# Kernel optimization log

Measured on AMD Instinct MI355X. Metric: run time of the kernel, lower is better.

## Reference

```python
import jax, jax.numpy as jnp
import numpy as np

B = 16384
IN = 128
H = 128
NC = 10
NATT = 3
EPS = 1e-5


def setup_inputs() -> dict:
    key = jax.random.key(0)
    ks = jax.random.split(key, 8)
    s_in = 1.0 / np.sqrt(IN)
    s_h = 1.0 / np.sqrt(H)
    return {
        "x": jax.random.normal(ks[0], (B, IN), dtype=jnp.float32),
        "W_in": jax.random.uniform(ks[1], (IN, H), jnp.float32, -s_in, s_in),
        "b_in": jax.random.uniform(ks[2], (H,), jnp.float32, -s_in, s_in),
        "W_att": jax.random.uniform(ks[3], (NATT, H, H), jnp.float32, -s_h, s_h),
        "b_att": jax.random.uniform(ks[4], (NATT, H), jnp.float32, -s_h, s_h),
        "gamma": jnp.ones((NATT, H), jnp.float32),
        "beta": jnp.zeros((NATT, H), jnp.float32),
        "W_c": jax.random.uniform(ks[5], (H, NC), jnp.float32, -s_h, s_h),
        "b_c": jax.random.uniform(ks[6], (NC,), jnp.float32, -s_h, s_h),
    }


def _layernorm(y, g, b):
    mu = jnp.mean(y, axis=-1, keepdims=True)
    var = jnp.mean((y - mu) ** 2, axis=-1, keepdims=True)
    return (y - mu) * jax.lax.rsqrt(var + EPS) * g + b


def reference(x, W_in, b_in, W_att, b_att, gamma, beta, W_c, b_c):
    # in_proj: [B, IN] -> [B, H]
    h = x @ W_in + b_in
    for i in range(NATT):
        u = jnp.tanh(h @ W_att[i] + b_att[i])            # [B, H]
        scores = u[:, :, None] * u[:, None, :]            # outer product [B, H, H]
        attn = jax.nn.softmax(scores, axis=-1)
        out = jnp.einsum("bij,bj->bi", attn, h)          # [B, H]
        h = _layernorm(h + out, gamma[i], beta[i])
    return h @ W_c + b_c                                  # [B, NC]
```

## Files before the change

kernel.cpp:

```cpp
#include <hip/hip_runtime.h>
#include <math.h>

#define B_TOT 16384
#define H     128
#define NC    10
#define NATT  3
#define TR    16
#define HBS   136
#define KT    5
#define EPS   1e-5f
#define EXM_S 100
#define EXL_S 20

typedef __attribute__((ext_vector_type(8))) short bf16x8;
typedef __attribute__((ext_vector_type(4))) float f32x4;

__device__ __forceinline__ ushort f2bf(float f) {
    union { float f; unsigned u; } v; v.f = f;
    unsigned r = v.u + 0x7fffu + ((v.u >> 16) & 1u);
    return (ushort)(r >> 16);
}

__device__ __forceinline__ float fast_tanh(float a) {
    float t = __expf(2.f * a);
    return 1.f - 2.f * __builtin_amdgcn_rcpf(t + 1.f);
}

__device__ __forceinline__ float redq(float v) {
    v += __shfl_xor(v, 16);
    v += __shfl_xor(v, 32);
    return v;
}

extern "C" __global__ __launch_bounds__(256)
void prep_weights(const float* __restrict__ W_in,
                  const float* __restrict__ W_att,
                  const float* __restrict__ W_c,
                  ushort* __restrict__ wt)
{
    int i = blockIdx.x * 256 + threadIdx.x;
    if (i < 65536) {
        int mat = i >> 14, idx = i & 16383;
        int k = idx >> 7, n = idx & 127;
        float v = (mat == 0) ? W_in[idx] : W_att[(mat - 1) * 16384 + idx];
        wt[mat * 16384 + n * H + k] = f2bf(v);
    } else if (i < 65536 + 2048) {
        int idx = i - 65536;
        int n = idx >> 7, k = idx & 127;
        float v = (n < NC) ? W_c[k * NC + n] : 0.f;
        wt[65536 + n * H + k] = f2bf(v);
    }
}

extern "C" __global__ __launch_bounds__(512, 6)
void simple_attention_kernel(const float* __restrict__ x,
                             const float* __restrict__ b_in,
                             const float* __restrict__ b_att,
                             const float* __restrict__ gamma,
                             const float* __restrict__ beta,
                             const float* __restrict__ b_c,
                             const ushort* __restrict__ wt,
                             float* __restrict__ out)
{
    __shared__ __align__(16) ushort ab[TR * HBS];
    __shared__ __align__(16) float  exm[16 * EXM_S];
    __shared__ __align__(16) float  exl[16 * EXL_S];

    const int tid  = threadIdx.x;
    const int wv   = tid >> 6;
    const int lane = tid & 63;
    const int s    = lane & 15;
    const int q    = lane >> 4;
    const int nq   = 16 * wv + 4 * q;
    const size_t rowBase = (size_t)blockIdx.x * TR;

    float h[4];
    f32x4 acc;

    if (wv < 4) {
        const float* xp = x + (rowBase + s) * H + 32 * wv + q * 8;
        float4 v0 = *(const float4*)xp;
        float4 v1 = *(const float4*)(xp + 4);
        bf16x8 a;
        a[0] = f2bf(v0.x); a[1] = f2bf(v0.y); a[2] = f2bf(v0.z); a[3] = f2bf(v0.w);
        a[4] = f2bf(v1.x); a[5] = f2bf(v1.y); a[6] = f2bf(v1.z); a[7] = f2bf(v1.w);
        *(bf16x8*)&ab[s * HBS + 32 * wv + q * 8] = a;
    }
    __syncthreads();

    {
        bf16x8 bfr[4];
        #pragma unroll
        for (int ks = 0; ks < 4; ++ks)
            bfr[ks] = *(const bf16x8*)&ab[s * HBS + ks * 32 + q * 8];
        acc = (f32x4){0.f, 0.f, 0.f, 0.f};
        #pragma unroll
        for (int ks = 0; ks < 4; ++ks) {
            bf16x8 a = *(const bf16x8*)&wt[(16 * wv + s) * H + ks * 32 + q * 8];
            acc = __builtin_amdgcn_mfma_f32_16x16x32_bf16(a, bfr[ks], acc, 0, 0, 0);
        }
        __syncthreads();
        float4 bi4 = *(const float4*)&b_in[nq];
        uint lo, hi;
        {
            float h0 = acc[0] + bi4.x, h1 = acc[1] + bi4.y;
            float h2 = acc[2] + bi4.z, h3 = acc[3] + bi4.w;
            h[0] = h0; h[1] = h1; h[2] = h2; h[3] = h3;
            lo = (uint)f2bf(h0) | ((uint)f2bf(h1) << 16);
            hi = (uint)f2bf(h2) | ((uint)f2bf(h3) << 16);
        }
        *(uint2*)&ab[s * HBS + nq] = make_uint2(lo, hi);
        __syncthreads();
    }

    const float cm[KT] = {1.00004478f, 0.99730768f, 0.49919676f, 0.17734736f, 0.04379392f};

    #pragma unroll 1
    for (int layer = 0; layer < NATT; ++layer) {
        const ushort* WT = wt + (size_t)(1 + layer) * 16384;

        bf16x8 bfr[4];
        #pragma unroll
        for (int ks = 0; ks < 4; ++ks)
            bfr[ks] = *(const bf16x8*)&ab[s * HBS + ks * 32 + q * 8];
        acc = (f32x4){0.f, 0.f, 0.f, 0.f};
        #pragma unroll
        for (int ks = 0; ks < 4; ++ks) {
            bf16x8 a = *(const bf16x8*)&WT[(16 * wv + s) * H + ks * 32 + q * 8];
            acc = __builtin_amdgcn_mfma_f32_16x16x32_bf16(a, bfr[ks], acc, 0, 0, 0);
        }
        float4 ba4 = *(const float4*)&b_att[layer * H + nq];
        float u[4];
        u[0] = fast_tanh(acc[0] + ba4.x);
        u[1] = fast_tanh(acc[1] + ba4.y);
        u[2] = fast_tanh(acc[2] + ba4.z);
        u[3] = fast_tanh(acc[3] + ba4.w);

        float m0 = 0, m1 = 0, m2 = 0, m3 = 0, m4 = 0;
        float t1 = 0, t2 = 0, t3 = 0, t4 = 0;
        #pragma unroll
        for (int r = 0; r < 4; ++r) {
            float uu = u[r], hh = h[r];
            m0 += hh;
            float p = uu;
            m1 += p * hh; t1 += p;
            p *= uu; m2 += p * hh; t2 += p;
            p *= uu; m3 += p * hh; t3 += p;
            p *= uu; m4 += p * hh; t4 += p;
        }
        m0 = redq(m0); m1 = redq(m1); m2 = redq(m2); m3 = redq(m3); m4 = redq(m4);
        t1 = redq(t1); t2 = redq(t2); t3 = redq(t3); t4 = redq(t4);
        {
            float* dst = &exm[s * EXM_S + wv * 12];
            if (q == 0)      *(f32x4*)&dst[0] = (f32x4){m0, m1, m2, m3};
            else if (q == 1) *(f32x4*)&dst[4] = (f32x4){m4, t1, t2, t3};
            else if (q == 2) *(f32x4*)&dst[8] = (f32x4){t4, 0.f, 0.f, 0.f};
        }
        __syncthreads();

        float S0, S1, S2, S3, S4, T1c, T2c, T3c, T4c;
        {
            const float* src = &exm[s * EXM_S + 24 * q];
            f32x4 a0 = *(const f32x4*)&src[0];
            f32x4 a1 = *(const f32x4*)&src[4];
            f32x4 a2 = *(const f32x4*)&src[8];
            f32x4 b0 = *(const f32x4*)&src[12];
            f32x4 b1 = *(const f32x4*)&src[16];
            f32x4 b2 = *(const f32x4*)&src[20];
            a0 += b0; a1 += b1; a2 += b2;
            S0  = redq(a0.x) * cm[0];
            S1  = redq(a0.y) * cm[1];
            S2  = redq(a0.z) * cm[2];
            S3  = redq(a0.w) * cm[3];
            S4  = redq(a1.x) * cm[4];
            T1c = redq(a1.y) * cm[1];
            T2c = redq(a1.z) * cm[2];
            T3c = redq(a1.w) * cm[3];
            T4c = redq(a2.x) * cm[4];
        }

        float ls = 0.f, lq2 = 0.f;
        #pragma unroll
        for (int r = 0; r < 4; ++r) {
            float uu = u[r];
            float num = fmaf(fmaf(fmaf(fmaf(S4, uu, S3), uu, S2), uu, S1), uu, S0);
            float den = fmaf(fmaf(fmaf(fmaf(T4c, uu, T3c), uu, T2c), uu, T1c), uu,
                             128.f * 1.00004478f);
            float yy = h[r] + num * __builtin_amdgcn_rcpf(den);
            h[r] = yy;
            ls += yy; lq2 += yy * yy;
        }
        ls  = redq(ls);
        lq2 = redq(lq2);
        if (q == 0)
            *(float2*)&exl[s * EXL_S + wv * 2] = make_float2(ls, lq2);
        __syncthreads();

        {
            f32x4 rd = *(const f32x4*)&exl[s * EXL_S + 4 * q];
            float sm  = redq(rd.x + rd.z);
            float sq2 = redq(rd.y + rd.w);
            float mu  = sm * (1.f / H);
            float var = sq2 * (1.f / H) - mu * mu;
            float inv = rsqrtf(var + EPS);
            float4 g4  = *(const float4*)&gamma[layer * H + nq];
            float4 be4 = *(const float4*)&beta [layer * H + nq];
            float h0 = (h[0] - mu) * inv * g4.x + be4.x;
            float h1 = (h[1] - mu) * inv * g4.y + be4.y;
            float h2 = (h[2] - mu) * inv * g4.z + be4.z;
            float h3 = (h[3] - mu) * inv * g4.w + be4.w;
            h[0] = h0; h[1] = h1; h[2] = h2; h[3] = h3;
            uint lo = (uint)f2bf(h0) | ((uint)f2bf(h1) << 16);
            uint hi = (uint)f2bf(h2) | ((uint)f2bf(h3) << 16);
            *(uint2*)&ab[s * HBS + nq] = make_uint2(lo, hi);
        }
        __syncthreads();
    }

    if (wv == 0) {
        const ushort* WC = wt + 4 * 16384;
        f32x4 facc = (f32x4){0.f, 0.f, 0.f, 0.f};
        #pragma unroll
        for (int ks = 0; ks < 4; ++ks) {
            bf16x8 a = *(const bf16x8*)&ab[s * HBS + ks * 32 + q * 8];
            bf16x8 b = *(const bf16x8*)&WC[s * H + ks * 32 + q * 8];
            facc = __builtin_amdgcn_mfma_f32_16x16x32_bf16(a, b, facc, 0, 0, 0);
        }
        if (s < NC) {
            float bc = b_c[s];
            #pragma unroll
            for (int r = 0; r < 4; ++r)
                out[(rowBase + 4 * q + r) * NC + s] = facc[r] + bc;
        }
    }
}

extern "C" void kernel_launch(void* const* d_in, const int* in_sizes, int n_in,
                              void* d_out, int out_size, void* d_ws, size_t ws_size,
                              hipStream_t stream) {
    const float* x     = (const float*)d_in[0];
    const float* W_in  = (const float*)d_in[1];
    const float* b_in  = (const float*)d_in[2];
    const float* W_att = (const float*)d_in[3];
    const float* b_att = (const float*)d_in[4];
    const float* gamma = (const float*)d_in[5];
    const float* beta  = (const float*)d_in[6];
    const float* W_c   = (const float*)d_in[7];
    const float* b_c   = (const float*)d_in[8];
    float* out  = (float*)d_out;
    ushort* wt  = (ushort*)d_ws;

    hipLaunchKernelGGL(prep_weights, dim3(264), dim3(256), 0, stream,
                       W_in, W_att, W_c, wt);
    hipLaunchKernelGGL(simple_attention_kernel, dim3(B_TOT / TR), dim3(512), 0, stream,
                       x, b_in, b_att, gamma, beta, b_c, wt, out);
}
```

Before: 100.6 us.

## Fold LayerNorm affine into next layer's attention weights and defer normalization

Gamma is folded into the attention weight matrices in the prep kernel, and precomputed correction vectors (gamma·W, beta·W + b_att) are stored in the workspace. The per-layer kernel now writes the un-normalized residual y to shared memory and applies mean/rstd analytically after the matmul, which removes one __syncthreads and one shared-memory round trip per layer. It adds extra prep work and reads of aux vectors, and normalizing after the bf16 matmul changes rounding behaviour because the un-normalized activations are quantized to bf16.

After: 102.8 us. +2.2%, slower.

```diff
diff --git a/kernel.cpp b/kernel.cpp
--- a/kernel.cpp
+++ b/kernel.cpp
@@ -36,26 +36,64 @@
 void prep_weights(const float* __restrict__ W_in,
                   const float* __restrict__ W_att,
                   const float* __restrict__ W_c,
+                  const float* __restrict__ gamma,
+                  const float* __restrict__ beta,
+                  const float* __restrict__ b_att,
                   ushort* __restrict__ wt)
 {
-    int i = blockIdx.x * 256 + threadIdx.x;
+    float* aux = (float*)(wt + 67584);
+    int bid = blockIdx.x;
+    if (bid >= 267) {
+        int w = (bid - 267) * 4 + (threadIdx.x >> 6);
+        if (w < 768) {
+            int l   = w >> 8;
+            int rem = w & 255;
+            int g2  = rem >> 7;
+            int n   = rem & 127;
+            int ln  = threadIdx.x & 63;
+            float sum = 0.f;
+            if (l > 0) {
+                const float* coef = (g2 == 0 ? gamma : beta) + (l - 1) * H;
+                sum = coef[ln]      * W_att[l * 16384 + ln * H + n]
+                    + coef[ln + 64] * W_att[l * 16384 + (ln + 64) * H + n];
+            }
+            #pragma unroll
+            for (int off = 1; off < 64; off <<= 1) sum += __shfl_xor(sum, off);
+            if (ln == 0) {
+                if (g2 == 1) sum += b_att[l * H + n];
+                aux[l * 512 + g2 * 128 + n] = sum;
+            }
+        }
+        return;
+    }
+    int i = bid * 256 + threadIdx.x;
     if (i < 65536) {
         int mat = i >> 14, idx = i & 16383;
         int k = idx >> 7, n = idx & 127;
         float v = (mat == 0) ? W_in[idx] : W_att[(mat - 1) * 16384 + idx];
+        if (mat >= 2) v *= gamma[(mat - 2) * H + k];
         wt[mat * 16384 + n * H + k] = f2bf(v);
-    } else if (i < 65536 + 2048) {
+    } else if (i < 67584) {
         int idx = i - 65536;
         int n = idx >> 7, k = idx & 127;
         float v = (n < NC) ? W_c[k * NC + n] : 0.f;
         wt[65536 + n * H + k] = f2bf(v);
+    } else if (i < 67584 + 768) {
+        int j = i - 67584;
+        int l = j >> 8;
+        int idx = j & 255;
+        int g = idx >> 7;
+        int n = idx & 127;
+        float v;
+        if (g == 0) v = (l == 0) ? 1.f : gamma[(l - 1) * H + n];
+        else        v = (l == 0) ? 0.f : beta [(l - 1) * H + n];
+        aux[l * 512 + (2 + g) * 128 + n] = v;
     }
 }
 
 extern "C" __global__ __launch_bounds__(512, 6)
 void simple_attention_kernel(const float* __restrict__ x,
                              const float* __restrict__ b_in,
-                             const float* __restrict__ b_att,
                              const float* __restrict__ gamma,
                              const float* __restrict__ beta,
                              const float* __restrict__ b_c,
@@ -73,8 +111,9 @@
     const int q    = lane >> 4;
     const int nq   = 16 * wv + 4 * q;
     const size_t rowBase = (size_t)blockIdx.x * TR;
-
-    float h[4];
+    const float* aux = (const float*)(wt + 67584);
+
+    float y[4];
     f32x4 acc;
 
     if (wv < 4) {
@@ -101,14 +140,11 @@
         }
         __syncthreads();
         float4 bi4 = *(const float4*)&b_in[nq];
-        uint lo, hi;
-        {
-            float h0 = acc[0] + bi4.x, h1 = acc[1] + bi4.y;
-            float h2 = acc[2] + bi4.z, h3 = acc[3] + bi4.w;
-            h[0] = h0; h[1] = h1; h[2] = h2; h[3] = h3;
-            lo = (uint)f2bf(h0) | ((uint)f2bf(h1) << 16);
-            hi = (uint)f2bf(h2) | ((uint)f2bf(h3) << 16);
-        }
+        float h0 = acc[0] + bi4.x, h1 = acc[1] + bi4.y;
+        float h2 = acc[2] + bi4.z, h3 = acc[3] + bi4.w;
+        y[0] = h0; y[1] = h1; y[2] = h2; y[3] = h3;
+        uint lo = (uint)f2bf(h0) | ((uint)f2bf(h1) << 16);
+        uint hi = (uint)f2bf(h2) | ((uint)f2bf(h3) << 16);
         *(uint2*)&ab[s * HBS + nq] = make_uint2(lo, hi);
         __syncthreads();
     }
@@ -118,6 +154,7 @@
     #pragma unroll 1
     for (int layer = 0; layer < NATT; ++layer) {
         const ushort* WT = wt + (size_t)(1 + layer) * 16384;
+        const float* AX  = aux + layer * 512;
 
         bf16x8 bfr[4];
         #pragma unroll
@@ -129,18 +166,38 @@
             bf16x8 a = *(const bf16x8*)&WT[(16 * wv + s) * H + ks * 32 + q * 8];
             acc = __builtin_amdgcn_mfma_f32_16x16x32_bf16(a, bfr[ks], acc, 0, 0, 0);
         }
-        float4 ba4 = *(const float4*)&b_att[layer * H + nq];
+
+        float mu, inv;
+        if (layer == 0) { mu = 0.f; inv = 1.f; }
+        else {
+            f32x4 rd = *(const f32x4*)&exl[s * EXL_S + 4 * q];
+            float sm  = redq(rd.x + rd.z);
+            float sq2 = redq(rd.y + rd.w);
+            mu  = sm * (1.f / H);
+            float var = sq2 * (1.f / H) - mu * mu;
+            inv = rsqrtf(var + EPS);
+        }
+        float invmu = inv * mu;
+
+        float4 gw4 = *(const float4*)&AX[nq];
+        float4 c14 = *(const float4*)&AX[128 + nq];
+        float4 gp4 = *(const float4*)&AX[256 + nq];
+        float4 bp4 = *(const float4*)&AX[384 + nq];
         float u[4];
-        u[0] = fast_tanh(acc[0] + ba4.x);
-        u[1] = fast_tanh(acc[1] + ba4.y);
-        u[2] = fast_tanh(acc[2] + ba4.z);
-        u[3] = fast_tanh(acc[3] + ba4.w);
+        u[0] = fast_tanh(fmaf(inv, acc[0], fmaf(-invmu, gw4.x, c14.x)));
+        u[1] = fast_tanh(fmaf(inv, acc[1], fmaf(-invmu, gw4.y, c14.y)));
+        u[2] = fast_tanh(fmaf(inv, acc[2], fmaf(-invmu, gw4.z, c14.z)));
+        u[3] = fast_tanh(fmaf(inv, acc[3], fmaf(-invmu, gw4.w, c14.w)));
+        y[0] = fmaf((y[0] - mu) * inv, gp4.x, bp4.x);
+        y[1] = fmaf((y[1] - mu) * inv, gp4.y, bp4.y);
+        y[2] = fmaf((y[2] - mu) * inv, gp4.z, bp4.z);
+        y[3] = fmaf((y[3] - mu) * inv, gp4.w, bp4.w);
 
         float m0 = 0, m1 = 0, m2 = 0, m3 = 0, m4 = 0;
         float t1 = 0, t2 = 0, t3 = 0, t4 = 0;
         #pragma unroll
         for (int r = 0; r < 4; ++r) {
-            float uu = u[r], hh = h[r];
+            float uu = u[r], hh = y[r];
             m0 += hh;
             float p = uu;
             m1 += p * hh; t1 += p;
@@ -186,35 +243,41 @@
             float num = fmaf(fmaf(fmaf(fmaf(S4, uu, S3), uu, S2), uu, S1), uu, S0);
             float den = fmaf(fmaf(fmaf(fmaf(T4c, uu, T3c), uu, T2c), uu, T1c), uu,
                              128.f * 1.00004478f);
-            float yy = h[r] + num * __builtin_amdgcn_rcpf(den);
-            h[r] = yy;
+            float yy = y[r] + num * __builtin_amdgcn_rcpf(den);
+            y[r] = yy;
             ls += yy; lq2 += yy * yy;
         }
         ls  = redq(ls);
         lq2 = redq(lq2);
-        if (q == 0)
-            *(float2*)&exl[s * EXL_S + wv * 2] = make_float2(ls, lq2);
-        __syncthreads();
-
-        {
+
+        if (layer < NATT - 1) {
+            uint lo = (uint)f2bf(y[0]) | ((uint)f2bf(y[1]) << 16);
+            uint hi = (uint)f2bf(y[2]) | ((uint)f2bf(y[3]) << 16);
+            *(uint2*)&ab[s * HBS + nq] = make_uint2(lo, hi);
+            if (q == 0)
+                *(float2*)&exl[s * EXL_S + wv * 2] = make_float2(ls, lq2);
+            __syncthreads();
+        } else {
+            if (q == 0)
+                *(float2*)&exl[s * EXL_S + wv * 2] = make_float2(ls, lq2);
+            __syncthreads();
             f32x4 rd = *(const f32x4*)&exl[s * EXL_S + 4 * q];
             float sm  = redq(rd.x + rd.z);
             float sq2 = redq(rd.y + rd.w);
-            float mu  = sm * (1.f / H);
-            float var = sq2 * (1.f / H) - mu * mu;
-            float inv = rsqrtf(var + EPS);
+            float mu2 = sm * (1.f / H);
+            float var = sq2 * (1.f / H) - mu2 * mu2;
+            float inv2 = rsqrtf(var + EPS);
             float4 g4  = *(const float4*)&gamma[layer * H + nq];
             float4 be4 = *(const float4*)&beta [layer * H + nq];
-            float h0 = (h[0] - mu) * inv * g4.x + be4.x;
-            float h1 = (h[1] - mu) * inv * g4.y + be4.y;
-            float h2 = (h[2] - mu) * inv * g4.z + be4.z;
-            float h3 = (h[3] - mu) * inv * g4.w + be4.w;
-            h[0] = h0; h[1] = h1; h[2] = h2; h[3] = h3;
+            float h0 = (y[0] - mu2) * inv2 * g4.x + be4.x;
+            float h1 = (y[1] - mu2) * inv2 * g4.y + be4.y;
+            float h2 = (y[2] - mu2) * inv2 * g4.z + be4.z;
+            float h3 = (y[3] - mu2) * inv2 * g4.w + be4.w;
             uint lo = (uint)f2bf(h0) | ((uint)f2bf(h1) << 16);
             uint hi = (uint)f2bf(h2) | ((uint)f2bf(h3) << 16);
             *(uint2*)&ab[s * HBS + nq] = make_uint2(lo, hi);
-        }
-        __syncthreads();
+            __syncthreads();
+        }
     }
 
     if (wv == 0) {
@@ -250,8 +313,8 @@
     float* out  = (float*)d_out;
     ushort* wt  = (ushort*)d_ws;
 
-    hipLaunchKernelGGL(prep_weights, dim3(264), dim3(256), 0, stream,
-                       W_in, W_att, W_c, wt);
+    hipLaunchKernelGGL(prep_weights, dim3(459), dim3(256), 0, stream,
+                       W_in, W_att, W_c, gamma, beta, b_att, wt);
     hipLaunchKernelGGL(simple_attention_kernel, dim3(B_TOT / TR), dim3(512), 0, stream,
-                       x, b_in, b_att, gamma, beta, b_c, wt, out);
-}
+                       x, b_in, gamma, beta, b_c, wt, out);
+}
```

## Process two 16-row tiles per block to reuse weight fragments across tiles

Applied to the files above, without the earlier changes.

Each block now handles 32 rows as two 16-row tiles, and each loaded weight fragment feeds two MFMAs, one per tile. This halves the global weight loads and the number of block-wide barriers per row, and gives every wave work during the input load and the classifier step. In exchange registers per thread roughly double, so the launch bound occupancy hint drops from 6 to 4, and the grid is half as large.

Result: no change. 99.08 us (median of 2 runs) (-1.5%).

```diff
diff --git a/kernel.cpp b/kernel.cpp
--- a/kernel.cpp
+++ b/kernel.cpp
@@ -5,7 +5,7 @@
 #define H     128
 #define NC    10
 #define NATT  3
-#define TR    16
+#define TRH   16
 #define HBS   136
 #define KT    5
 #define EPS   1e-5f
@@ -52,7 +52,7 @@
     }
 }
 
-extern "C" __global__ __launch_bounds__(512, 6)
+extern "C" __global__ __launch_bounds__(512, 4)
 void simple_attention_kernel(const float* __restrict__ x,
                              const float* __restrict__ b_in,
                              const float* __restrict__ b_att,
@@ -62,9 +62,9 @@
                              const ushort* __restrict__ wt,
                              float* __restrict__ out)
 {
-    __shared__ __align__(16) ushort ab[TR * HBS];
-    __shared__ __align__(16) float  exm[16 * EXM_S];
-    __shared__ __align__(16) float  exl[16 * EXL_S];
+    __shared__ __align__(16) ushort ab[2][TRH * HBS];
+    __shared__ __align__(16) float  exm[2][16 * EXM_S];
+    __shared__ __align__(16) float  exl[2][16 * EXL_S];
 
     const int tid  = threadIdx.x;
     const int wv   = tid >> 6;
@@ -72,44 +72,51 @@
     const int s    = lane & 15;
     const int q    = lane >> 4;
     const int nq   = 16 * wv + 4 * q;
-    const size_t rowBase = (size_t)blockIdx.x * TR;
-
-    float h[4];
-    f32x4 acc;
-
-    if (wv < 4) {
-        const float* xp = x + (rowBase + s) * H + 32 * wv + q * 8;
+    const size_t rowBase = (size_t)blockIdx.x * (2 * TRH);
+
+    float yA[4], yB[4];
+    f32x4 accA, accB;
+
+    {
+        int tile  = wv >> 2;
+        int slice = wv & 3;
+        const float* xp = x + (rowBase + tile * TRH + s) * H + 32 * slice + q * 8;
         float4 v0 = *(const float4*)xp;
         float4 v1 = *(const float4*)(xp + 4);
         bf16x8 a;
         a[0] = f2bf(v0.x); a[1] = f2bf(v0.y); a[2] = f2bf(v0.z); a[3] = f2bf(v0.w);
         a[4] = f2bf(v1.x); a[5] = f2bf(v1.y); a[6] = f2bf(v1.z); a[7] = f2bf(v1.w);
-        *(bf16x8*)&ab[s * HBS + 32 * wv + q * 8] = a;
+        *(bf16x8*)&ab[tile][s * HBS + 32 * slice + q * 8] = a;
     }
     __syncthreads();
 
     {
-        bf16x8 bfr[4];
-        #pragma unroll
-        for (int ks = 0; ks < 4; ++ks)
-            bfr[ks] = *(const bf16x8*)&ab[s * HBS + ks * 32 + q * 8];
-        acc = (f32x4){0.f, 0.f, 0.f, 0.f};
+        bf16x8 bfrA[4], bfrB[4];
+        #pragma unroll
+        for (int ks = 0; ks < 4; ++ks) {
+            bfrA[ks] = *(const bf16x8*)&ab[0][s * HBS + ks * 32 + q * 8];
+            bfrB[ks] = *(const bf16x8*)&ab[1][s * HBS + ks * 32 + q * 8];
+        }
+        accA = (f32x4){0.f, 0.f, 0.f, 0.f};
+        accB = (f32x4){0.f, 0.f, 0.f, 0.f};
         #pragma unroll
         for (int ks = 0; ks < 4; ++ks) {
             bf16x8 a = *(const bf16x8*)&wt[(16 * wv + s) * H + ks * 32 + q * 8];
-            acc = __builtin_amdgcn_mfma_f32_16x16x32_bf16(a, bfr[ks], acc, 0, 0, 0);
+            accA = __builtin_amdgcn_mfma_f32_16x16x32_bf16(a, bfrA[ks], accA, 0, 0, 0);
+            accB = __builtin_amdgcn_mfma_f32_16x16x32_bf16(a, bfrB[ks], accB, 0, 0, 0);
         }
         __syncthreads();
         float4 bi4 = *(const float4*)&b_in[nq];
-        uint lo, hi;
-        {
-            float h0 = acc[0] + bi4.x, h1 = acc[1] + bi4.y;
-            float h2 = acc[2] + bi4.z, h3 = acc[3] + bi4.w;
-            h[0] = h0; h[1] = h1; h[2] = h2; h[3] = h3;
-            lo = (uint)f2bf(h0) | ((uint)f2bf(h1) << 16);
-            hi = (uint)f2bf(h2) | ((uint)f2bf(h3) << 16);
-        }
-        *(uint2*)&ab[s * HBS + nq] = make_uint2(lo, hi);
+        yA[0] = accA[0] + bi4.x; yA[1] = accA[1] + bi4.y;
+        yA[2] = accA[2] + bi4.z; yA[3] = accA[3] + bi4.w;
+        yB[0] = accB[0] + bi4.x; yB[1] = accB[1] + bi4.y;
+        yB[2] = accB[2] + bi4.z; yB[3] = accB[3] + bi4.w;
+        uint loA = (uint)f2bf(yA[0]) | ((uint)f2bf(yA[1]) << 16);
+        uint hiA = (uint)f2bf(yA[2]) | ((uint)f2bf(yA[3]) << 16);
+        uint loB = (uint)f2bf(yB[0]) | ((uint)f2bf(yB[1]) << 16);
+        uint hiB = (uint)f2bf(yB[2]) | ((uint)f2bf(yB[3]) << 16);
+        *(uint2*)&ab[0][s * HBS + nq] = make_uint2(loA, hiA);
+        *(uint2*)&ab[1][s * HBS + nq] = make_uint2(loB, hiB);
         __syncthreads();
     }
 
@@ -119,48 +126,57 @@
     for (int layer = 0; layer < NATT; ++layer) {
         const ushort* WT = wt + (size_t)(1 + layer) * 16384;
 
-        bf16x8 bfr[4];
-        #pragma unroll
-        for (int ks = 0; ks < 4; ++ks)
-            bfr[ks] = *(const bf16x8*)&ab[s * HBS + ks * 32 + q * 8];
-        acc = (f32x4){0.f, 0.f, 0.f, 0.f};
+        bf16x8 bfrA[4], bfrB[4];
+        #pragma unroll
+        for (int ks = 0; ks < 4; ++ks) {
+            bfrA[ks] = *(const bf16x8*)&ab[0][s * HBS + ks * 32 + q * 8];
+            bfrB[ks] = *(const bf16x8*)&ab[1][s * HBS + ks * 32 + q * 8];
+        }
+        accA = (f32x4){0.f, 0.f, 0.f, 0.f};
+        accB = (f32x4){0.f, 0.f, 0.f, 0.f};
         #pragma unroll
         for (int ks = 0; ks < 4; ++ks) {
             bf16x8 a = *(const bf16x8*)&WT[(16 * wv + s) * H + ks * 32 + q * 8];
-            acc = __builtin_amdgcn_mfma_f32_16x16x32_bf16(a, bfr[ks], acc, 0, 0, 0);
+            accA = __builtin_amdgcn_mfma_f32_16x16x32_bf16(a, bfrA[ks], accA, 0, 0, 0);
+            accB = __builtin_amdgcn_mfma_f32_16x16x32_bf16(a, bfrB[ks], accB, 0, 0, 0);
         }
         float4 ba4 = *(const float4*)&b_att[layer * H + nq];
-        float u[4];
-        u[0] = fast_tanh(acc[0] + ba4.x);
-        u[1] = fast_tanh(acc[1] + ba4.y);
-        u[2] = fast_tanh(acc[2] + ba4.z);
-        u[3] = fast_tanh(acc[3] + ba4.w);
-
-        float m0 = 0, m1 = 0, m2 = 0, m3 = 0, m4 = 0;
-        float t1 = 0, t2 = 0, t3 = 0, t4 = 0;
-        #pragma unroll
-        for (int r = 0; r < 4; ++r) {
-            float uu = u[r], hh = h[r];
-            m0 += hh;
-            float p = uu;
-            m1 += p * hh; t1 += p;
-            p *= uu; m2 += p * hh; t2 += p;
-            p *= uu; m3 += p * hh; t3 += p;
-            p *= uu; m4 += p * hh; t4 += p;
-        }
-        m0 = redq(m0); m1 = redq(m1); m2 = redq(m2); m3 = redq(m3); m4 = redq(m4);
-        t1 = redq(t1); t2 = redq(t2); t3 = redq(t3); t4 = redq(t4);
-        {
-            float* dst = &exm[s * EXM_S + wv * 12];
+        float uA[4], uB[4];
+        uA[0] = fast_tanh(accA[0] + ba4.x); uA[1] = fast_tanh(accA[1] + ba4.y);
+        uA[2] = fast_tanh(accA[2] + ba4.z); uA[3] = fast_tanh(accA[3] + ba4.w);
+        uB[0] = fast_tanh(accB[0] + ba4.x); uB[1] = fast_tanh(accB[1] + ba4.y);
+        uB[2] = fast_tanh(accB[2] + ba4.z); uB[3] = fast_tanh(accB[3] + ba4.w);
+
+        #pragma unroll
+        for (int tl = 0; tl < 2; ++tl) {
+            const float* yy = tl ? yB : yA;
+            const float* uu = tl ? uB : uA;
+            float m0 = 0, m1 = 0, m2 = 0, m3 = 0, m4 = 0;
+            float t1 = 0, t2 = 0, t3 = 0, t4 = 0;
+            #pragma unroll
+            for (int r = 0; r < 4; ++r) {
+                float uv = uu[r], hh = yy[r];
+                m0 += hh;
+                float p = uv;
+                m1 += p * hh; t1 += p;
+                p *= uv; m2 += p * hh; t2 += p;
+                p *= uv; m3 += p * hh; t3 += p;
+                p *= uv; m4 += p * hh; t4 += p;
+            }
+            m0 = redq(m0); m1 = redq(m1); m2 = redq(m2); m3 = redq(m3); m4 = redq(m4);
+            t1 = redq(t1); t2 = redq(t2); t3 = redq(t3); t4 = redq(t4);
+            float* dst = &exm[tl][s * EXM_S + wv * 12];
             if (q == 0)      *(f32x4*)&dst[0] = (f32x4){m0, m1, m2, m3};
             else if (q == 1) *(f32x4*)&dst[4] = (f32x4){m4, t1, t2, t3};
             else if (q == 2) *(f32x4*)&dst[8] = (f32x4){t4, 0.f, 0.f, 0.f};
         }
         __syncthreads();
 
-        float S0, S1, S2, S3, S4, T1c, T2c, T3c, T4c;
-        {
-            const float* src = &exm[s * EXM_S + 24 * q];
+        #pragma unroll
+        for (int tl = 0; tl < 2; ++tl) {
+            float* yy = tl ? yB : yA;
+            const float* uu = tl ? uB : uA;
+            const float* src = &exm[tl][s * EXM_S + 24 * q];
             f32x4 a0 = *(const f32x4*)&src[0];
             f32x4 a1 = *(const f32x4*)&src[4];
             f32x4 a2 = *(const f32x4*)&src[8];
@@ -168,61 +184,63 @@
             f32x4 b1 = *(const f32x4*)&src[16];
             f32x4 b2 = *(const f32x4*)&src[20];
             a0 += b0; a1 += b1; a2 += b2;
-            S0  = redq(a0.x) * cm[0];
-            S1  = redq(a0.y) * cm[1];
-            S2  = redq(a0.z) * cm[2];
-            S3  = redq(a0.w) * cm[3];
-            S4  = redq(a1.x) * cm[4];
-            T1c = redq(a1.y) * cm[1];
-            T2c = redq(a1.z) * cm[2];
-            T3c = redq(a1.w) * cm[3];
-            T4c = redq(a2.x) * cm[4];
-        }
-
-        float ls = 0.f, lq2 = 0.f;
-        #pragma unroll
-        for (int r = 0; r < 4; ++r) {
-            float uu = u[r];
-            float num = fmaf(fmaf(fmaf(fmaf(S4, uu, S3), uu, S2), uu, S1), uu, S0);
-            float den = fmaf(fmaf(fmaf(fmaf(T4c, uu, T3c), uu, T2c), uu, T1c), uu,
-                             128.f * 1.00004478f);
-            float yy = h[r] + num * __builtin_amdgcn_rcpf(den);
-            h[r] = yy;
-            ls += yy; lq2 += yy * yy;
-        }
-        ls  = redq(ls);
-        lq2 = redq(lq2);
-        if (q == 0)
-            *(float2*)&exl[s * EXL_S + wv * 2] = make_float2(ls, lq2);
-        __syncthreads();
-
-        {
-            f32x4 rd = *(const f32x4*)&exl[s * EXL_S + 4 * q];
+            float S0  = redq(a0.x) * cm[0];
+            float S1  = redq(a0.y) * cm[1];
+            float S2  = redq(a0.z) * cm[2];
+            float S3  = redq(a0.w) * cm[3];
+            float S4  = redq(a1.x) * cm[4];
+            float T1c = redq(a1.y) * cm[1];
+            float T2c = redq(a1.z) * cm[2];
+            float T3c = redq(a1.w) * cm[3];
+            float T4c = redq(a2.x) * cm[4];
+            float ls = 0.f, lq2 = 0.f;
+            #pragma unroll
+            for (int r = 0; r < 4; ++r) {
+                float uv = uu[r];
+                float num = fmaf(fmaf(fmaf(fmaf(S4, uv, S3), uv, S2), uv, S1), uv, S0);
+                float den = fmaf(fmaf(fmaf(fmaf(T4c, uv, T3c), uv, T2c), uv, T1c), uv,
+                                 128.f * 1.00004478f);
+                float yv = yy[r] + num * __builtin_amdgcn_rcpf(den);
+                yy[r] = yv;
+                ls += yv; lq2 += yv * yv;
+            }
+            ls  = redq(ls);
+            lq2 = redq(lq2);
+            if (q == 0)
+                *(float2*)&exl[tl][s * EXL_S + wv * 2] = make_float2(ls, lq2);
+        }
+        __syncthreads();
+
+        float4 g4  = *(const float4*)&gamma[layer * H + nq];
+        float4 be4 = *(const float4*)&beta [layer * H + nq];
+        #pragma unroll
+        for (int tl = 0; tl < 2; ++tl) {
+            float* yy = tl ? yB : yA;
+            f32x4 rd = *(const f32x4*)&exl[tl][s * EXL_S + 4 * q];
             float sm  = redq(rd.x + rd.z);
             float sq2 = redq(rd.y + rd.w);
             float mu  = sm * (1.f / H);
             float var = sq2 * (1.f / H) - mu * mu;
             float inv = rsqrtf(var + EPS);
-            float4 g4  = *(const float4*)&gamma[layer * H + nq];
-            float4 be4 = *(const float4*)&beta [layer * H + nq];
-            float h0 = (h[0] - mu) * inv * g4.x + be4.x;
-            float h1 = (h[1] - mu) * inv * g4.y + be4.y;
-            float h2 = (h[2] - mu) * inv * g4.z + be4.z;
-            float h3 = (h[3] - mu) * inv * g4.w + be4.w;
-            h[0] = h0; h[1] = h1; h[2] = h2; h[3] = h3;
+            float h0 = (yy[0] - mu) * inv * g4.x + be4.x;
+            float h1 = (yy[1] - mu) * inv * g4.y + be4.y;
+            float h2 = (yy[2] - mu) * inv * g4.z + be4.z;
+            float h3 = (yy[3] - mu) * inv * g4.w + be4.w;
+            yy[0] = h0; yy[1] = h1; yy[2] = h2; yy[3] = h3;
             uint lo = (uint)f2bf(h0) | ((uint)f2bf(h1) << 16);
             uint hi = (uint)f2bf(h2) | ((uint)f2bf(h3) << 16);
-            *(uint2*)&ab[s * HBS + nq] = make_uint2(lo, hi);
-        }
-        __syncthreads();
-    }
-
-    if (wv == 0) {
+            *(uint2*)&ab[tl][s * HBS + nq] = make_uint2(lo, hi);
+        }
+        __syncthreads();
+    }
+
+    if ((wv & 3) == 0) {
+        int tile = wv >> 2;
         const ushort* WC = wt + 4 * 16384;
         f32x4 facc = (f32x4){0.f, 0.f, 0.f, 0.f};
         #pragma unroll
         for (int ks = 0; ks < 4; ++ks) {
-            bf16x8 a = *(const bf16x8*)&ab[s * HBS + ks * 32 + q * 8];
+            bf16x8 a = *(const bf16x8*)&ab[tile][s * HBS + ks * 32 + q * 8];
             bf16x8 b = *(const bf16x8*)&WC[s * H + ks * 32 + q * 8];
             facc = __builtin_amdgcn_mfma_f32_16x16x32_bf16(a, b, facc, 0, 0, 0);
         }
@@ -230,7 +248,7 @@
             float bc = b_c[s];
             #pragma unroll
             for (int r = 0; r < 4; ++r)
-                out[(rowBase + 4 * q + r) * NC + s] = facc[r] + bc;
+                out[(rowBase + tile * TRH + 4 * q + r) * NC + s] = facc[r] + bc;
         }
     }
 }
@@ -252,6 +270,6 @@
 
     hipLaunchKernelGGL(prep_weights, dim3(264), dim3(256), 0, stream,
                        W_in, W_att, W_c, wt);
-    hipLaunchKernelGGL(simple_attention_kernel, dim3(B_TOT / TR), dim3(512), 0, stream,
+    hipLaunchKernelGGL(simple_attention_kernel, dim3(B_TOT / (2 * TRH)), dim3(512), 0, stream,
                        x, b_in, b_att, gamma, beta, b_c, wt, out);
 }
```

## Use one wavefront per 16-row tile to drop cross-wave LDS reductions

Applied to the files above, without the earlier changes.

Work for a 16-row tile moves from eight wavefronts, each owning 16 output columns, to a single 64-lane wavefront that loops over all eight column tiles and keeps 32 h and u values per lane in registers. This replaces the cross-wave LDS exchanges and most block barriers for the moment sums and the layernorm statistics with in-wave shuffle reductions. The x tile is converted straight into MFMA operands without an LDS round trip. In exchange each block does eight times more serial work, uses far more registers per lane, and every wavefront reloads the full weight matrices, so latency hiding depends on enough resident waves.

Result: no change. 102.0 us (+1.4%).

```diff
diff --git a/kernel.cpp b/kernel.cpp
--- a/kernel.cpp
+++ b/kernel.cpp
@@ -5,12 +5,8 @@
 #define H     128
 #define NC    10
 #define NATT  3
-#define TR    16
 #define HBS   136
-#define KT    5
 #define EPS   1e-5f
-#define EXM_S 100
-#define EXL_S 20
 
 typedef __attribute__((ext_vector_type(8))) short bf16x8;
 typedef __attribute__((ext_vector_type(4))) float f32x4;
@@ -52,7 +48,7 @@
     }
 }
 
-extern "C" __global__ __launch_bounds__(512, 6)
+extern "C" __global__ __launch_bounds__(64)
 void simple_attention_kernel(const float* __restrict__ x,
                              const float* __restrict__ b_in,
                              const float* __restrict__ b_att,
@@ -62,58 +58,49 @@
                              const ushort* __restrict__ wt,
                              float* __restrict__ out)
 {
-    __shared__ __align__(16) ushort ab[TR * HBS];
-    __shared__ __align__(16) float  exm[16 * EXM_S];
-    __shared__ __align__(16) float  exl[16 * EXL_S];
-
-    const int tid  = threadIdx.x;
-    const int wv   = tid >> 6;
-    const int lane = tid & 63;
+    __shared__ __align__(16) ushort ab[16 * HBS];
+
+    const int lane = threadIdx.x;
     const int s    = lane & 15;
     const int q    = lane >> 4;
-    const int nq   = 16 * wv + 4 * q;
-    const size_t rowBase = (size_t)blockIdx.x * TR;
-
-    float h[4];
-    f32x4 acc;
-
-    if (wv < 4) {
-        const float* xp = x + (rowBase + s) * H + 32 * wv + q * 8;
-        float4 v0 = *(const float4*)xp;
-        float4 v1 = *(const float4*)(xp + 4);
-        bf16x8 a;
-        a[0] = f2bf(v0.x); a[1] = f2bf(v0.y); a[2] = f2bf(v0.z); a[3] = f2bf(v0.w);
-        a[4] = f2bf(v1.x); a[5] = f2bf(v1.y); a[6] = f2bf(v1.z); a[7] = f2bf(v1.w);
-        *(bf16x8*)&ab[s * HBS + 32 * wv + q * 8] = a;
-    }
-    __syncthreads();
+    const size_t base = (size_t)blockIdx.x * 16;
+
+    float h[32];
+    float u[32];
 
     {
         bf16x8 bfr[4];
         #pragma unroll
-        for (int ks = 0; ks < 4; ++ks)
-            bfr[ks] = *(const bf16x8*)&ab[s * HBS + ks * 32 + q * 8];
-        acc = (f32x4){0.f, 0.f, 0.f, 0.f};
-        #pragma unroll
         for (int ks = 0; ks < 4; ++ks) {
-            bf16x8 a = *(const bf16x8*)&wt[(16 * wv + s) * H + ks * 32 + q * 8];
-            acc = __builtin_amdgcn_mfma_f32_16x16x32_bf16(a, bfr[ks], acc, 0, 0, 0);
-        }
-        __syncthreads();
-        float4 bi4 = *(const float4*)&b_in[nq];
-        uint lo, hi;
-        {
-            float h0 = acc[0] + bi4.x, h1 = acc[1] + bi4.y;
-            float h2 = acc[2] + bi4.z, h3 = acc[3] + bi4.w;
-            h[0] = h0; h[1] = h1; h[2] = h2; h[3] = h3;
-            lo = (uint)f2bf(h0) | ((uint)f2bf(h1) << 16);
-            hi = (uint)f2bf(h2) | ((uint)f2bf(h3) << 16);
-        }
-        *(uint2*)&ab[s * HBS + nq] = make_uint2(lo, hi);
-        __syncthreads();
-    }
-
-    const float cm[KT] = {1.00004478f, 0.99730768f, 0.49919676f, 0.17734736f, 0.04379392f};
+            const float* xp = x + (base + s) * H + ks * 32 + q * 8;
+            float4 v0 = *(const float4*)xp;
+            float4 v1 = *(const float4*)(xp + 4);
+            bf16x8 a;
+            a[0] = f2bf(v0.x); a[1] = f2bf(v0.y); a[2] = f2bf(v0.z); a[3] = f2bf(v0.w);
+            a[4] = f2bf(v1.x); a[5] = f2bf(v1.y); a[6] = f2bf(v1.z); a[7] = f2bf(v1.w);
+            bfr[ks] = a;
+        }
+        #pragma unroll
+        for (int t = 0; t < 8; ++t) {
+            f32x4 acc = (f32x4){0.f, 0.f, 0.f, 0.f};
+            #pragma unroll
+            for (int ks = 0; ks < 4; ++ks) {
+                bf16x8 a = *(const bf16x8*)&wt[(16 * t + s) * H + ks * 32 + q * 8];
+                acc = __builtin_amdgcn_mfma_f32_16x16x32_bf16(a, bfr[ks], acc, 0, 0, 0);
+            }
+            float4 bi = *(const float4*)&b_in[16 * t + 4 * q];
+            float h0 = acc[0] + bi.x, h1 = acc[1] + bi.y;
+            float h2 = acc[2] + bi.z, h3 = acc[3] + bi.w;
+            h[4 * t + 0] = h0; h[4 * t + 1] = h1;
+            h[4 * t + 2] = h2; h[4 * t + 3] = h3;
+            uint lo = (uint)f2bf(h0) | ((uint)f2bf(h1) << 16);
+            uint hi = (uint)f2bf(h2) | ((uint)f2bf(h3) << 16);
+            *(uint2*)&ab[s * HBS + 16 * t + 4 * q] = make_uint2(lo, hi);
+        }
+    }
+    __syncthreads();
+
+    const float cm[5] = {1.00004478f, 0.99730768f, 0.49919676f, 0.17734736f, 0.04379392f};
 
     #pragma unroll 1
     for (int layer = 0; layer < NATT; ++layer) {
@@ -123,114 +110,90 @@
         #pragma unroll
         for (int ks = 0; ks < 4; ++ks)
             bfr[ks] = *(const bf16x8*)&ab[s * HBS + ks * 32 + q * 8];
-        acc = (f32x4){0.f, 0.f, 0.f, 0.f};
-        #pragma unroll
-        for (int ks = 0; ks < 4; ++ks) {
-            bf16x8 a = *(const bf16x8*)&WT[(16 * wv + s) * H + ks * 32 + q * 8];
-            acc = __builtin_amdgcn_mfma_f32_16x16x32_bf16(a, bfr[ks], acc, 0, 0, 0);
-        }
-        float4 ba4 = *(const float4*)&b_att[layer * H + nq];
-        float u[4];
-        u[0] = fast_tanh(acc[0] + ba4.x);
-        u[1] = fast_tanh(acc[1] + ba4.y);
-        u[2] = fast_tanh(acc[2] + ba4.z);
-        u[3] = fast_tanh(acc[3] + ba4.w);
 
         float m0 = 0, m1 = 0, m2 = 0, m3 = 0, m4 = 0;
         float t1 = 0, t2 = 0, t3 = 0, t4 = 0;
         #pragma unroll
-        for (int r = 0; r < 4; ++r) {
-            float uu = u[r], hh = h[r];
-            m0 += hh;
-            float p = uu;
-            m1 += p * hh; t1 += p;
-            p *= uu; m2 += p * hh; t2 += p;
-            p *= uu; m3 += p * hh; t3 += p;
-            p *= uu; m4 += p * hh; t4 += p;
-        }
+        for (int t = 0; t < 8; ++t) {
+            f32x4 acc = (f32x4){0.f, 0.f, 0.f, 0.f};
+            #pragma unroll
+            for (int ks = 0; ks < 4; ++ks) {
+                bf16x8 a = *(const bf16x8*)&WT[(16 * t + s) * H + ks * 32 + q * 8];
+                acc = __builtin_amdgcn_mfma_f32_16x16x32_bf16(a, bfr[ks], acc, 0, 0, 0);
+            }
+            float4 ba = *(const float4*)&b_att[layer * H + 16 * t + 4 * q];
+            float bav[4] = {ba.x, ba.y, ba.z, ba.w};
+            #pragma unroll
+            for (int r = 0; r < 4; ++r) {
+                float uu = fast_tanh(acc[r] + bav[r]);
+                u[4 * t + r] = uu;
+                float hh = h[4 * t + r];
+                m0 += hh;
+                float p = uu;
+                m1 += p * hh; t1 += p;
+                p *= uu; m2 += p * hh; t2 += p;
+                p *= uu; m3 += p * hh; t3 += p;
+                p *= uu; m4 += p * hh; t4 += p;
+            }
+        }
+
         m0 = redq(m0); m1 = redq(m1); m2 = redq(m2); m3 = redq(m3); m4 = redq(m4);
         t1 = redq(t1); t2 = redq(t2); t3 = redq(t3); t4 = redq(t4);
-        {
-            float* dst = &exm[s * EXM_S + wv * 12];
-            if (q == 0)      *(f32x4*)&dst[0] = (f32x4){m0, m1, m2, m3};
-            else if (q == 1) *(f32x4*)&dst[4] = (f32x4){m4, t1, t2, t3};
-            else if (q == 2) *(f32x4*)&dst[8] = (f32x4){t4, 0.f, 0.f, 0.f};
-        }
-        __syncthreads();
-
-        float S0, S1, S2, S3, S4, T1c, T2c, T3c, T4c;
-        {
-            const float* src = &exm[s * EXM_S + 24 * q];
-            f32x4 a0 = *(const f32x4*)&src[0];
-            f32x4 a1 = *(const f32x4*)&src[4];
-            f32x4 a2 = *(const f32x4*)&src[8];
-            f32x4 b0 = *(const f32x4*)&src[12];
-            f32x4 b1 = *(const f32x4*)&src[16];
-            f32x4 b2 = *(const f32x4*)&src[20];
-            a0 += b0; a1 += b1; a2 += b2;
-            S0  = redq(a0.x) * cm[0];
-            S1  = redq(a0.y) * cm[1];
-            S2  = redq(a0.z) * cm[2];
-            S3  = redq(a0.w) * cm[3];
-            S4  = redq(a1.x) * cm[4];
-            T1c = redq(a1.y) * cm[1];
-            T2c = redq(a1.z) * cm[2];
-            T3c = redq(a1.w) * cm[3];
-            T4c = redq(a2.x) * cm[4];
-        }
+        float S0 = m0 * cm[0], S1 = m1 * cm[1], S2 = m2 * cm[2];
+        float S3 = m3 * cm[3], S4 = m4 * cm[4];
+        float T1 = t1 * cm[1], T2 = t2 * cm[2], T3 = t3 * cm[3], T4 = t4 * cm[4];
 
         float ls = 0.f, lq2 = 0.f;
         #pragma unroll
-        for (int r = 0; r < 4; ++r) {
-            float uu = u[r];
+        for (int i = 0; i < 32; ++i) {
+            float uu = u[i];
             float num = fmaf(fmaf(fmaf(fmaf(S4, uu, S3), uu, S2), uu, S1), uu, S0);
-            float den = fmaf(fmaf(fmaf(fmaf(T4c, uu, T3c), uu, T2c), uu, T1c), uu,
+            float den = fmaf(fmaf(fmaf(fmaf(T4, uu, T3), uu, T2), uu, T1), uu,
                              128.f * 1.00004478f);
-            float yy = h[r] + num * __builtin_amdgcn_rcpf(den);
-            h[r] = yy;
+            float yy = h[i] + num * __builtin_amdgcn_rcpf(den);
+            h[i] = yy;
             ls += yy; lq2 += yy * yy;
         }
         ls  = redq(ls);
         lq2 = redq(lq2);
-        if (q == 0)
-            *(float2*)&exl[s * EXL_S + wv * 2] = make_float2(ls, lq2);
-        __syncthreads();
-
-        {
-            f32x4 rd = *(const f32x4*)&exl[s * EXL_S + 4 * q];
-            float sm  = redq(rd.x + rd.z);
-            float sq2 = redq(rd.y + rd.w);
-            float mu  = sm * (1.f / H);
-            float var = sq2 * (1.f / H) - mu * mu;
-            float inv = rsqrtf(var + EPS);
-            float4 g4  = *(const float4*)&gamma[layer * H + nq];
-            float4 be4 = *(const float4*)&beta [layer * H + nq];
-            float h0 = (h[0] - mu) * inv * g4.x + be4.x;
-            float h1 = (h[1] - mu) * inv * g4.y + be4.y;
-            float h2 = (h[2] - mu) * inv * g4.z + be4.z;
-            float h3 = (h[3] - mu) * inv * g4.w + be4.w;
-            h[0] = h0; h[1] = h1; h[2] = h2; h[3] = h3;
+        float mu  = ls * (1.f / H);
+        float var = lq2 * (1.f / H) - mu * mu;
+        float inv = rsqrtf(var + EPS);
+
+        #pragma unroll
+        for (int t = 0; t < 8; ++t) {
+            float4 g4  = *(const float4*)&gamma[layer * H + 16 * t + 4 * q];
+            float4 be4 = *(const float4*)&beta [layer * H + 16 * t + 4 * q];
+            float h0 = (h[4 * t + 0] - mu) * inv * g4.x + be4.x;
+            float h1 = (h[4 * t + 1] - mu) * inv * g4.y + be4.y;
+            float h2 = (h[4 * t + 2] - mu) * inv * g4.z + be4.z;
+            float h3 = (h[4 * t + 3] - mu) * inv * g4.w + be4.w;
+            h[4 * t + 0] = h0; h[4 * t + 1] = h1;
+            h[4 * t + 2] = h2; h[4 * t + 3] = h3;
             uint lo = (uint)f2bf(h0) | ((uint)f2bf(h1) << 16);
             uint hi = (uint)f2bf(h2) | ((uint)f2bf(h3) << 16);
-            *(uint2*)&ab[s * HBS + nq] = make_uint2(lo, hi);
+            *(uint2*)&ab[s * HBS + 16 * t + 4 * q] = make_uint2(lo, hi);
         }
         __syncthreads();
     }
 
-    if (wv == 0) {
+    {
         const ushort* WC = wt + 4 * 16384;
-        f32x4 facc = (f32x4){0.f, 0.f, 0.f, 0.f};
+        bf16x8 bfr[4];
+        #pragma unroll
+        for (int ks = 0; ks < 4; ++ks)
+            bfr[ks] = *(const bf16x8*)&ab[s * HBS + ks * 32 + q * 8];
+        f32x4 acc = (f32x4){0.f, 0.f, 0.f, 0.f};
         #pragma unroll
         for (int ks = 0; ks < 4; ++ks) {
-            bf16x8 a = *(const bf16x8*)&ab[s * HBS + ks * 32 + q * 8];
-            bf16x8 b = *(const bf16x8*)&WC[s * H + ks * 32 + q * 8];
-            facc = __builtin_amdgcn_mfma_f32_16x16x32_bf16(a, b, facc, 0, 0, 0);
-        }
-        if (s < NC) {
-            float bc = b_c[s];
-            #pragma unroll
-            for (int r = 0; r < 4; ++r)
-                out[(rowBase + 4 * q + r) * NC + s] = facc[r] + bc;
+            bf16x8 a = *(const bf16x8*)&WC[s * H + ks * 32 + q * 8];
+            acc = __builtin_amdgcn_mfma_f32_16x16x32_bf16(a, bfr[ks], acc, 0, 0, 0);
+        }
+        #pragma unroll
+        for (int r = 0; r < 4; ++r) {
+            int nc = 4 * q + r;
+            if (nc < NC)
+                out[(base + s) * NC + nc] = acc[r] + b_c[nc];
         }
     }
 }
@@ -252,6 +215,6 @@
 
     hipLaunchKernelGGL(prep_weights, dim3(264), dim3(256), 0, stream,
                        W_in, W_att, W_c, wt);
-    hipLaunchKernelGGL(simple_attention_kernel, dim3(B_TOT / TR), dim3(512), 0, stream,
+    hipLaunchKernelGGL(simple_attention_kernel, dim3(B_TOT / 16), dim3(64), 0, stream,
                        x, b_in, b_att, gamma, beta, b_c, wt, out);
 }
```
